# Performance work log

Measured on AMD Instinct MI355X. Metric: run time of the kernel, lower is better.

The kernel has to match this reference:

```python
import jax, jax.numpy as jnp
import numpy as np

# Static problem structure (matches setup_inputs)
B, NPOLY, VPP, L = 32, 256, 64, 32
LAYERS = 3
PLEN = L * 2 ** LAYERS  # 256
LN_EPS = 1e-5


def _layernorm(h, g, b):
    mu = h.mean(-1, keepdims=True)
    var = ((h - mu) ** 2).mean(-1, keepdims=True)
    return g * (h - mu) / jnp.sqrt(var + LN_EPS) + b


def _forward(data, W0, b0, g0, beta0, W1, b1, g1, beta1, W2, b2, g2, beta2,
             Wq, bq, Wk, bk, Wv, bv):
    # row 0 holds agent polyline index in feature 0
    agent_id = data[:, 0, 0].astype(jnp.int32)  # [B]
    vecs = data[:, 1:, :]
    vecs = vecs.at[:, :, -1].set(0.0)  # zero out polyline-id feature (data[:,:,-1]=0)
    x = vecs.reshape(B, NPOLY, VPP, L)  # uniform polyline groups

    # SubGraph: 3 layers of (MLP -> maxpool aggregate -> concat), doubling width
    for (W, b, g, be) in ((W0, b0, g0, beta0), (W1, b1, g1, beta1), (W2, b2, g2, beta2)):
        h = jax.nn.relu(_layernorm(x @ W + b, g, be))  # [B,P,V,c]
        agg = h.max(axis=2, keepdims=True)             # [B,P,1,c]
        x = jnp.concatenate([h, jnp.broadcast_to(agg, h.shape)], axis=-1)  # [B,P,V,2c]
    P = x.max(axis=2)  # [B, NPOLY, PLEN] polyline features

    # Global graph: single-head attention with agent polyline as query
    q = P[jnp.arange(B), agent_id] @ Wq + bq          # [B, C]
    k = P @ Wk + bk                                    # [B, P, C]
    v = P @ Wv + bv
    scores = jnp.einsum('bc,bpc->bp', q, k) / jnp.sqrt(jnp.float32(PLEN))
    att = jax.nn.softmax(scores, axis=-1)
    return jnp.einsum('bp,bpc->bc', att, v)           # [B, PLEN]


def setup_inputs() -> dict:
    key = jax.random.key(0)
    ks = jax.random.split(key, 24)
    V = 1 + NPOLY * VPP
    data = jax.random.normal(ks[0], (B, V, L), dtype=jnp.float32)
    agent = jax.random.randint(ks[1], (B,), 0, NPOLY).astype(jnp.float32)
    data = data.at[:, 0, :].set(0.0).at[:, 0, 0].set(agent)
    pid = jnp.repeat(jnp.arange(NPOLY), VPP).astype(jnp.float32)
    data = data.at[:, 1:, -1].set(pid[None, :])

    inp = {'data': data}
    c = L
    for i in range(LAYERS):
        inp[f'W{i}'] = 0.02 * jax.random.normal(ks[2 + i], (c, c), dtype=jnp.float32)
        inp[f'b{i}'] = jnp.zeros((c,), jnp.float32)
        inp[f'g{i}'] = jnp.ones((c,), jnp.float32)
        inp[f'beta{i}'] = jnp.zeros((c,), jnp.float32)
        c *= 2
    C = PLEN
    for j, nm in enumerate(('q', 'k', 'v')):
        inp[f'W{nm}'] = 0.02 * jax.random.normal(ks[10 + j], (C, C), dtype=jnp.float32)
        inp[f'b{nm}'] = jnp.zeros((C,), jnp.float32)
    return inp


def reference(data, W0, b0, g0, beta0, W1, b1, g1, beta1, W2, b2, g2, beta2,
              Wq, bq, Wk, bk, Wv, bv):
    return _forward(data, W0, b0, g0, beta0, W1, b1, g1, beta1, W2, b2, g2, beta2,
                    Wq, bq, Wk, bk, Wv, bv)
```

## Files before the change

### kernel.cpp

```cpp
#include <hip/hip_runtime.h>

#define NPOLY 256
#define VPP   64
#define LCH   32
#define NV    (1 + NPOLY * VPP)
#define LN_EPS 1e-5f

typedef __bf16 bf16x8 __attribute__((ext_vector_type(8)));
typedef float  f32x4  __attribute__((ext_vector_type(4)));

union U4B8 { uint4 u; bf16x8 v; };

__device__ __forceinline__ unsigned f2bf_u(float f) {
    unsigned u = __float_as_uint(f);
    return (u + 0x7FFFu + ((u >> 16) & 1u)) >> 16;
}
__device__ __forceinline__ unsigned packbf(float a, float b) {
    return f2bf_u(a) | (f2bf_u(b) << 16);
}

__global__ void vn_prep1(const float* __restrict__ W0, const float* __restrict__ W1,
                         const float* __restrict__ W2,
                         const float* __restrict__ Wq, const float* __restrict__ Wk,
                         const float* __restrict__ Wv,
                         float* __restrict__ Wqf, float* __restrict__ Wkf,
                         float* __restrict__ Wvf, uint4* __restrict__ wpack)
{
    int t = blockIdx.x * 256 + threadIdx.x;
    if (t < 3 * 32768) {
        int which = t >> 15, r = t & 32767;
        const float* src = which == 0 ? Wq : which == 1 ? Wk : Wv;
        float*       dst = which == 0 ? Wqf : which == 1 ? Wkf : Wvf;
        dst[r] = src[r] + src[r + 128 * 256];
        return;
    }
    t -= 3 * 32768;
    if (t >= 22 * 64) return;
    int f = t >> 6, L = t & 63, q = L >> 4, m = L & 15;
    const float* src; int N, k0, col;
    if (f < 2)      { src = W0; N = 32;  k0 = q * 8;                 col = f * 16 + m; }
    else if (f < 6) { src = W1; N = 64;  k0 = q * 8;                 col = (f - 2) * 16 + m; }
    else { int g = f - 6; src = W2; N = 128; k0 = (g >> 3) * 32 + q * 8; col = (g & 7) * 16 + m; }
    float e[8];
    #pragma unroll
    for (int j = 0; j < 8; j++) e[j] = src[(k0 + j) * N + col];
    uint4 o;
    o.x = packbf(e[0], e[1]); o.y = packbf(e[2], e[3]);
    o.z = packbf(e[4], e[5]); o.w = packbf(e[6], e[7]);
    wpack[f * 64 + L] = o;
}

__global__ void vn_prep2(const float* __restrict__ Wqf, const float* __restrict__ Wkf,
                         const float* __restrict__ bq,
                         float* __restrict__ Mff, float* __restrict__ u0f)
{
    int t = blockIdx.x * 256 + threadIdx.x;
    if (t < 16384) {
        int i = t >> 7, j = t & 127;
        const float* a = Wqf + i * 256;
        const float* b = Wkf + j * 256;
        float s = 0.f;
        for (int c = 0; c < 256; c++) s = fmaf(a[c], b[c], s);
        Mff[i * 128 + j] = s;
    } else if (t < 16512) {
        int j = t - 16384;
        const float* b = Wkf + j * 256;
        float s = 0.f;
        for (int c = 0; c < 256; c++) s = fmaf(bq[c], b[c], s);
        u0f[j] = s;
    }
}

__global__ __launch_bounds__(64, 2) void vn_mlp(
    const float* __restrict__ data, const uint4* __restrict__ wpack,
    const float* __restrict__ b0, const float* __restrict__ g0, const float* __restrict__ be0,
    const float* __restrict__ W1, const float* __restrict__ b1,
    const float* __restrict__ g1, const float* __restrict__ be1,
    const float* __restrict__ W2, const float* __restrict__ b2,
    const float* __restrict__ g2, const float* __restrict__ be2,
    float* __restrict__ Ph)
{
    __shared__ __align__(16) unsigned short hbuf[64 * 72];
    __shared__ float fbuf[192];

    const int blk = blockIdx.x;
    const int L = threadIdx.x, q = L >> 4, m = L & 15;
    const int bb = blk >> 8, pp = blk & 255;

    const float* rowbase = data + ((size_t)bb * NV + 1 + (size_t)pp * VPP) * LCH;
    bf16x8 A0[4];
    #pragma unroll
    for (int rt = 0; rt < 4; rt++) {
        const float* rp = rowbase + (size_t)(rt * 16 + m) * LCH + q * 8;
        float4 u = *(const float4*)rp;
        float4 v = *(const float4*)(rp + 4);
        if (q == 3) v.w = 0.f;
        U4B8 c;
        c.u.x = packbf(u.x, u.y); c.u.y = packbf(u.z, u.w);
        c.u.z = packbf(v.x, v.y); c.u.w = packbf(v.z, v.w);
        A0[rt] = c.v;
    }
    U4B8 t0, t1; t0.u = wpack[0 * 64 + L]; t1.u = wpack[1 * 64 + L];
    float bc0[2] = { b0[m], b0[16 + m] };
    f32x4 acc0[4][2];
    #pragma unroll
    for (int rt = 0; rt < 4; rt++) {
        {
            f32x4 a = { bc0[0], bc0[0], bc0[0], bc0[0] };
            acc0[rt][0] = __builtin_amdgcn_mfma_f32_16x16x32_bf16(A0[rt], t0.v, a, 0, 0, 0);
        }
        {
            f32x4 a = { bc0[1], bc0[1], bc0[1], bc0[1] };
            acc0[rt][1] = __builtin_amdgcn_mfma_f32_16x16x32_bf16(A0[rt], t1.v, a, 0, 0, 0);
        }
    }
    float g0c[2]  = { g0[m],  g0[16 + m]  };
    float be0c[2] = { be0[m], be0[16 + m] };
    float a0mx[2] = { 0.f, 0.f };
    #pragma unroll
    for (int rt = 0; rt < 4; rt++) {
        #pragma unroll
        for (int reg = 0; reg < 4; reg++) {
            float x0 = acc0[rt][0][reg], x1 = acc0[rt][1][reg];
            float rs = x0 + x1, rq = x0 * x0 + x1 * x1;
            #pragma unroll
            for (int s = 1; s < 16; s <<= 1) { rs += __shfl_xor(rs, s, 64); rq += __shfl_xor(rq, s, 64); }
            float mu = rs * (1.f / 32.f);
            float var = rq * (1.f / 32.f) - mu * mu;
            float ri = rsqrtf(var + LN_EPS);
            #pragma unroll
            for (int ct = 0; ct < 2; ct++) {
                float v = fmaxf(fmaf(g0c[ct] * ri, acc0[rt][ct][reg] - mu, be0c[ct]), 0.f);
                acc0[rt][ct][reg] = v;
                a0mx[ct] = fmaxf(a0mx[ct], v);
            }
        }
    }
    #pragma unroll
    for (int ct = 0; ct < 2; ct++) {
        float v = a0mx[ct];
        v = fmaxf(v, __shfl_xor(v, 16, 64));
        v = fmaxf(v, __shfl_xor(v, 32, 64));
        a0mx[ct] = v;
    }
    if (q == 0) { fbuf[m] = a0mx[0]; fbuf[16 + m] = a0mx[1]; }
    __syncthreads();
    float au1 = b1[L];
    for (int j = 0; j < 32; j++)
        au1 = fmaf(fbuf[j], W1[(32 + j) * 64 + L], au1);
    #pragma unroll
    for (int rt = 0; rt < 4; rt++)
        #pragma unroll
        for (int reg = 0; reg < 4; reg++) {
            int row = rt * 16 + q * 4 + reg;
            hbuf[row * 72 + m]      = (unsigned short)f2bf_u(acc0[rt][0][reg]);
            hbuf[row * 72 + 16 + m] = (unsigned short)f2bf_u(acc0[rt][1][reg]);
        }
    __syncthreads();
    fbuf[64 + L] = au1;
    __syncthreads();

    bf16x8 A1[4];
    #pragma unroll
    for (int rt = 0; rt < 4; rt++) {
        U4B8 c; c.u = *(const uint4*)(hbuf + (rt * 16 + m) * 72 + q * 8);
        A1[rt] = c.v;
    }
    f32x4 acc1[4][4];
    #pragma unroll
    for (int ct = 0; ct < 4; ct++) {
        U4B8 w; w.u = wpack[(2 + ct) * 64 + L];
        float au = fbuf[64 + ct * 16 + m];
        #pragma unroll
        for (int rt = 0; rt < 4; rt++) {
            f32x4 a = { au, au, au, au };
            acc1[rt][ct] = __builtin_amdgcn_mfma_f32_16x16x32_bf16(A1[rt], w.v, a, 0, 0, 0);
        }
    }
    float g1c[4], be1c[4];
    #pragma unroll
    for (int ct = 0; ct < 4; ct++) { g1c[ct] = g1[ct * 16 + m]; be1c[ct] = be1[ct * 16 + m]; }
    float a1mx[4] = { 0.f, 0.f, 0.f, 0.f };
    #pragma unroll
    for (int rt = 0; rt < 4; rt++) {
        #pragma unroll
        for (int reg = 0; reg < 4; reg++) {
            float rs = 0.f, rq = 0.f;
            #pragma unroll
            for (int ct = 0; ct < 4; ct++) { float x = acc1[rt][ct][reg]; rs += x; rq += x * x; }
            #pragma unroll
            for (int s = 1; s < 16; s <<= 1) { rs += __shfl_xor(rs, s, 64); rq += __shfl_xor(rq, s, 64); }
            float mu = rs * (1.f / 64.f);
            float var = rq * (1.f / 64.f) - mu * mu;
            float ri = rsqrtf(var + LN_EPS);
            #pragma unroll
            for (int ct = 0; ct < 4; ct++) {
                float v = fmaxf(fmaf(g1c[ct] * ri, acc1[rt][ct][reg] - mu, be1c[ct]), 0.f);
                acc1[rt][ct][reg] = v;
                a1mx[ct] = fmaxf(a1mx[ct], v);
            }
        }
    }
    #pragma unroll
    for (int ct = 0; ct < 4; ct++) {
        float v = a1mx[ct];
        v = fmaxf(v, __shfl_xor(v, 16, 64));
        v = fmaxf(v, __shfl_xor(v, 32, 64));
        a1mx[ct] = v;
    }
    __syncthreads();
    if (q == 0) {
        #pragma unroll
        for (int ct = 0; ct < 4; ct++) fbuf[ct * 16 + m] = a1mx[ct];
    }
    __syncthreads();
    float au2a = b2[L], au2b = b2[64 + L];
    for (int j = 0; j < 64; j++) {
        float av = fbuf[j];
        au2a = fmaf(av, W2[(64 + j) * 128 + L],      au2a);
        au2b = fmaf(av, W2[(64 + j) * 128 + 64 + L], au2b);
    }
    #pragma unroll
    for (int rt = 0; rt < 4; rt++)
        #pragma unroll
        for (int reg = 0; reg < 4; reg++) {
            int row = rt * 16 + q * 4 + reg;
            #pragma unroll
            for (int ct = 0; ct < 4; ct++)
                hbuf[row * 72 + ct * 16 + m] = (unsigned short)f2bf_u(acc1[rt][ct][reg]);
        }
    __syncthreads();
    fbuf[64 + L] = au2a; fbuf[128 + L] = au2b;
    __syncthreads();

    bf16x8 A2[4][2];
    #pragma unroll
    for (int rt = 0; rt < 4; rt++)
        #pragma unroll
        for (int ks = 0; ks < 2; ks++) {
            U4B8 c; c.u = *(const uint4*)(hbuf + (rt * 16 + m) * 72 + ks * 32 + q * 8);
            A2[rt][ks] = c.v;
        }
    f32x4 acc2[8][4];
    #pragma unroll
    for (int ct = 0; ct < 8; ct++) {
        U4B8 wa, wb;
        wa.u = wpack[(6 + ct) * 64 + L];
        wb.u = wpack[(14 + ct) * 64 + L];
        float au = fbuf[64 + ct * 16 + m];
        #pragma unroll
        for (int rt = 0; rt < 4; rt++) {
            f32x4 a = { au, au, au, au };
            a = __builtin_amdgcn_mfma_f32_16x16x32_bf16(A2[rt][0], wa.v, a, 0, 0, 0);
            a = __builtin_amdgcn_mfma_f32_16x16x32_bf16(A2[rt][1], wb.v, a, 0, 0, 0);
            acc2[ct][rt] = a;
        }
    }
    float g2c[8], be2c[8];
    #pragma unroll
    for (int ct = 0; ct < 8; ct++) { g2c[ct] = g2[ct * 16 + m]; be2c[ct] = be2[ct * 16 + m]; }
    float m2[8] = { 0.f, 0.f, 0.f, 0.f, 0.f, 0.f, 0.f, 0.f };
    #pragma unroll
    for (int rt = 0; rt < 4; rt++) {
        #pragma unroll
        for (int reg = 0; reg < 4; reg++) {
            float rs = 0.f, rq = 0.f;
            #pragma unroll
            for (int ct = 0; ct < 8; ct++) { float x = acc2[ct][rt][reg]; rs += x; rq += x * x; }
            #pragma unroll
            for (int s = 1; s < 16; s <<= 1) { rs += __shfl_xor(rs, s, 64); rq += __shfl_xor(rq, s, 64); }
            float mu = rs * (1.f / 128.f);
            float var = rq * (1.f / 128.f) - mu * mu;
            float ri = rsqrtf(var + LN_EPS);
            #pragma unroll
            for (int ct = 0; ct < 8; ct++) {
                float v = fmaxf(fmaf(g2c[ct] * ri, acc2[ct][rt][reg] - mu, be2c[ct]), 0.f);
                m2[ct] = fmaxf(m2[ct], v);
            }
        }
    }
    #pragma unroll
    for (int ct = 0; ct < 8; ct++) {
        float v = m2[ct];
        v = fmaxf(v, __shfl_xor(v, 16, 64));
        v = fmaxf(v, __shfl_xor(v, 32, 64));
        m2[ct] = v;
    }
    float v1 = q == 0 ? m2[0] : q == 1 ? m2[1] : q == 2 ? m2[2] : m2[3];
    float v2 = q == 0 ? m2[4] : q == 1 ? m2[5] : q == 2 ? m2[6] : m2[7];
    float* op = Ph + (size_t)blk * 128;
    op[L] = v1; op[64 + L] = v2;
}

__global__ __launch_bounds__(256) void vn_attn(
    const float* __restrict__ data, const float* __restrict__ Ph,
    const float* __restrict__ Mff, const float* __restrict__ u0f,
    const float* __restrict__ Wvf, const float* __restrict__ bv,
    float* __restrict__ out)
{
    __shared__ float pah[128], tts[128], sc[256], pb[128], red[8];
    const int b = blockIdx.x, tid = threadIdx.x, lane = tid & 63, wave = tid >> 6;
    const float* PhB = Ph + (size_t)b * NPOLY * 128;
    const int agent = (int)data[(size_t)b * NV * LCH];

    if (tid < 128) pah[tid] = PhB[(size_t)agent * 128 + tid];
    __syncthreads();
    if (tid < 128) {
        float a = u0f[tid];
        for (int i = 0; i < 128; i++) a = fmaf(pah[i], Mff[i * 128 + tid], a);
        tts[tid] = a;
    }
    __syncthreads();
    for (int pi = 0; pi < 64; pi++) {
        const int p = wave * 64 + pi;
        const float* pr = PhB + (size_t)p * 128;
        float s = pr[lane] * tts[lane];
        s = fmaf(pr[64 + lane], tts[64 + lane], s);
        #pragma unroll
        for (int st = 1; st < 64; st <<= 1) s += __shfl_xor(s, st, 64);
        if (lane == 0) sc[p] = s * 0.0625f;
    }
    __syncthreads();
    float sv = sc[tid];
    float mx = sv;
    #pragma unroll
    for (int s = 1; s < 64; s <<= 1) mx = fmaxf(mx, __shfl_xor(mx, s, 64));
    if (lane == 0) red[wave] = mx;
    __syncthreads();
    mx = fmaxf(fmaxf(red[0], red[1]), fmaxf(red[2], red[3]));
    float e = expf(sv - mx);
    float sm = e;
    #pragma unroll
    for (int s = 1; s < 64; s <<= 1) sm += __shfl_xor(sm, s, 64);
    if (lane == 0) red[4 + wave] = sm;
    __syncthreads();
    const float tot = red[4] + red[5] + red[6] + red[7];
    sc[tid] = e / tot;
    __syncthreads();
    if (tid < 128) {
        float a = 0.f;
        for (int p = 0; p < 256; p++) a = fmaf(sc[p], PhB[(size_t)p * 128 + tid], a);
        pb[tid] = a;
    }
    __syncthreads();
    float o = bv[tid];
    for (int j = 0; j < 128; j++) o = fmaf(pb[j], Wvf[j * 256 + tid], o);
    out[(size_t)b * 256 + tid] = o;
}

extern "C" void kernel_launch(void* const* d_in, const int* in_sizes, int n_in,
                              void* d_out, int out_size, void* d_ws, size_t ws_size,
                              hipStream_t stream)
{
    const float* data = (const float*)d_in[0];
    const float* W0 = (const float*)d_in[1];
    const float* b0 = (const float*)d_in[2];
    const float* g0 = (const float*)d_in[3];
    const float* be0= (const float*)d_in[4];
    const float* W1 = (const float*)d_in[5];
    const float* b1 = (const float*)d_in[6];
    const float* g1 = (const float*)d_in[7];
    const float* be1= (const float*)d_in[8];
    const float* W2 = (const float*)d_in[9];
    const float* b2 = (const float*)d_in[10];
    const float* g2 = (const float*)d_in[11];
    const float* be2= (const float*)d_in[12];
    const float* Wq = (const float*)d_in[13];
    const float* bq = (const float*)d_in[14];
    const float* Wk = (const float*)d_in[15];
    const float* bk = (const float*)d_in[16];
    const float* Wv = (const float*)d_in[17];
    const float* bv = (const float*)d_in[18];
    (void)bk;

    char* wsb = (char*)d_ws;
    float* Ph    = (float*)(wsb);
    float* Wqf   = (float*)(wsb + 4194304);
    float* Wkf   = (float*)(wsb + 4325376);
    float* Wvf   = (float*)(wsb + 4456448);
    float* Mff   = (float*)(wsb + 4587520);
    float* u0f   = (float*)(wsb + 4653056);
    uint4* wpack = (uint4*)(wsb + 4653568);

    vn_prep1<<<390, 256, 0, stream>>>(W0, W1, W2, Wq, Wk, Wv, Wqf, Wkf, Wvf, wpack);
    vn_prep2<<<65, 256, 0, stream>>>(Wqf, Wkf, bq, Mff, u0f);
    vn_mlp<<<32 * NPOLY, 64, 0, stream>>>(data, wpack,
                                          b0, g0, be0,
                                          W1, b1, g1, be1,
                                          W2, b2, g2, be2, Ph);
    vn_attn<<<32, 256, 0, stream>>>(data, Ph, Mff, u0f, Wvf, bv, (float*)d_out);
}
```

Measured before the change: 233.5 us.

## Pack four polylines per MLP block and drop the Wq·Wk precompute kernel

```diff
diff --git a/kernel.cpp b/kernel.cpp
--- a/kernel.cpp
+++ b/kernel.cpp
@@ -50,28 +50,7 @@
     wpack[f * 64 + L] = o;
 }
 
-__global__ void vn_prep2(const float* __restrict__ Wqf, const float* __restrict__ Wkf,
-                         const float* __restrict__ bq,
-                         float* __restrict__ Mff, float* __restrict__ u0f)
-{
-    int t = blockIdx.x * 256 + threadIdx.x;
-    if (t < 16384) {
-        int i = t >> 7, j = t & 127;
-        const float* a = Wqf + i * 256;
-        const float* b = Wkf + j * 256;
-        float s = 0.f;
-        for (int c = 0; c < 256; c++) s = fmaf(a[c], b[c], s);
-        Mff[i * 128 + j] = s;
-    } else if (t < 16512) {
-        int j = t - 16384;
-        const float* b = Wkf + j * 256;
-        float s = 0.f;
-        for (int c = 0; c < 256; c++) s = fmaf(bq[c], b[c], s);
-        u0f[j] = s;
-    }
-}
-
-__global__ __launch_bounds__(64, 2) void vn_mlp(
+__global__ __launch_bounds__(256) void vn_mlp(
     const float* __restrict__ data, const uint4* __restrict__ wpack,
     const float* __restrict__ b0, const float* __restrict__ g0, const float* __restrict__ be0,
     const float* __restrict__ W1, const float* __restrict__ b1,
@@ -80,12 +59,16 @@
     const float* __restrict__ g2, const float* __restrict__ be2,
     float* __restrict__ Ph)
 {
-    __shared__ __align__(16) unsigned short hbuf[64 * 72];
-    __shared__ float fbuf[192];
-
-    const int blk = blockIdx.x;
-    const int L = threadIdx.x, q = L >> 4, m = L & 15;
+    __shared__ __align__(16) unsigned short hbuf[4][64 * 72];
+    __shared__ float fbuf[4][192];
+
+    const int w = threadIdx.x >> 6;
+    const int L = threadIdx.x & 63, q = L >> 4, m = L & 15;
+    const int blk = blockIdx.x * 4 + w;
     const int bb = blk >> 8, pp = blk & 255;
+
+    unsigned short* hb = hbuf[w];
+    float* fb = fbuf[w];
 
     const float* rowbase = data + ((size_t)bb * NV + 1 + (size_t)pp * VPP) * LCH;
     bf16x8 A0[4];
@@ -143,38 +126,35 @@
         v = fmaxf(v, __shfl_xor(v, 32, 64));
         a0mx[ct] = v;
     }
-    if (q == 0) { fbuf[m] = a0mx[0]; fbuf[16 + m] = a0mx[1]; }
-    __syncthreads();
+    if (q == 0) { fb[m] = a0mx[0]; fb[16 + m] = a0mx[1]; }
     float au1 = b1[L];
     for (int j = 0; j < 32; j++)
-        au1 = fmaf(fbuf[j], W1[(32 + j) * 64 + L], au1);
+        au1 = fmaf(fb[j], W1[(32 + j) * 64 + L], au1);
     #pragma unroll
     for (int rt = 0; rt < 4; rt++)
         #pragma unroll
         for (int reg = 0; reg < 4; reg++) {
             int row = rt * 16 + q * 4 + reg;
-            hbuf[row * 72 + m]      = (unsigned short)f2bf_u(acc0[rt][0][reg]);
-            hbuf[row * 72 + 16 + m] = (unsigned short)f2bf_u(acc0[rt][1][reg]);
-        }
-    __syncthreads();
-    fbuf[64 + L] = au1;
-    __syncthreads();
+            hb[row * 72 + m]      = (unsigned short)f2bf_u(acc0[rt][0][reg]);
+            hb[row * 72 + 16 + m] = (unsigned short)f2bf_u(acc0[rt][1][reg]);
+        }
+    fb[64 + L] = au1;
 
     bf16x8 A1[4];
     #pragma unroll
     for (int rt = 0; rt < 4; rt++) {
-        U4B8 c; c.u = *(const uint4*)(hbuf + (rt * 16 + m) * 72 + q * 8);
+        U4B8 c; c.u = *(const uint4*)(hb + (rt * 16 + m) * 72 + q * 8);
         A1[rt] = c.v;
     }
     f32x4 acc1[4][4];
     #pragma unroll
     for (int ct = 0; ct < 4; ct++) {
-        U4B8 w; w.u = wpack[(2 + ct) * 64 + L];
-        float au = fbuf[64 + ct * 16 + m];
+        U4B8 wv; wv.u = wpack[(2 + ct) * 64 + L];
+        float au = fb[64 + ct * 16 + m];
         #pragma unroll
         for (int rt = 0; rt < 4; rt++) {
             f32x4 a = { au, au, au, au };
-            acc1[rt][ct] = __builtin_amdgcn_mfma_f32_16x16x32_bf16(A1[rt], w.v, a, 0, 0, 0);
+            acc1[rt][ct] = __builtin_amdgcn_mfma_f32_16x16x32_bf16(A1[rt], wv.v, a, 0, 0, 0);
         }
     }
     float g1c[4], be1c[4];
@@ -208,15 +188,13 @@
         v = fmaxf(v, __shfl_xor(v, 32, 64));
         a1mx[ct] = v;
     }
-    __syncthreads();
     if (q == 0) {
         #pragma unroll
-        for (int ct = 0; ct < 4; ct++) fbuf[ct * 16 + m] = a1mx[ct];
-    }
-    __syncthreads();
+        for (int ct = 0; ct < 4; ct++) fb[ct * 16 + m] = a1mx[ct];
+    }
     float au2a = b2[L], au2b = b2[64 + L];
     for (int j = 0; j < 64; j++) {
-        float av = fbuf[j];
+        float av = fb[j];
         au2a = fmaf(av, W2[(64 + j) * 128 + L],      au2a);
         au2b = fmaf(av, W2[(64 + j) * 128 + 64 + L], au2b);
     }
@@ -227,18 +205,16 @@
             int row = rt * 16 + q * 4 + reg;
             #pragma unroll
             for (int ct = 0; ct < 4; ct++)
-                hbuf[row * 72 + ct * 16 + m] = (unsigned short)f2bf_u(acc1[rt][ct][reg]);
-        }
-    __syncthreads();
-    fbuf[64 + L] = au2a; fbuf[128 + L] = au2b;
-    __syncthreads();
+                hb[row * 72 + ct * 16 + m] = (unsigned short)f2bf_u(acc1[rt][ct][reg]);
+        }
+    fb[64 + L] = au2a; fb[128 + L] = au2b;
 
     bf16x8 A2[4][2];
     #pragma unroll
     for (int rt = 0; rt < 4; rt++)
         #pragma unroll
         for (int ks = 0; ks < 2; ks++) {
-            U4B8 c; c.u = *(const uint4*)(hbuf + (rt * 16 + m) * 72 + ks * 32 + q * 8);
+            U4B8 c; c.u = *(const uint4*)(hb + (rt * 16 + m) * 72 + ks * 32 + q * 8);
             A2[rt][ks] = c.v;
         }
     f32x4 acc2[8][4];
@@ -247,7 +223,7 @@
         U4B8 wa, wb;
         wa.u = wpack[(6 + ct) * 64 + L];
         wb.u = wpack[(14 + ct) * 64 + L];
-        float au = fbuf[64 + ct * 16 + m];
+        float au = fb[64 + ct * 16 + m];
         #pragma unroll
         for (int rt = 0; rt < 4; rt++) {
             f32x4 a = { au, au, au, au };
@@ -294,21 +270,33 @@
 
 __global__ __launch_bounds__(256) void vn_attn(
     const float* __restrict__ data, const float* __restrict__ Ph,
-    const float* __restrict__ Mff, const float* __restrict__ u0f,
-    const float* __restrict__ Wvf, const float* __restrict__ bv,
-    float* __restrict__ out)
+    const float* __restrict__ Wqf, const float* __restrict__ Wkf,
+    const float* __restrict__ Wvf, const float* __restrict__ bq,
+    const float* __restrict__ bv, float* __restrict__ out)
 {
-    __shared__ float pah[128], tts[128], sc[256], pb[128], red[8];
+    __shared__ float pah[128], qs[256], tts[128], sc[256], pb[128], red[8];
     const int b = blockIdx.x, tid = threadIdx.x, lane = tid & 63, wave = tid >> 6;
     const float* PhB = Ph + (size_t)b * NPOLY * 128;
     const int agent = (int)data[(size_t)b * NV * LCH];
 
     if (tid < 128) pah[tid] = PhB[(size_t)agent * 128 + tid];
     __syncthreads();
-    if (tid < 128) {
-        float a = u0f[tid];
-        for (int i = 0; i < 128; i++) a = fmaf(pah[i], Mff[i * 128 + tid], a);
-        tts[tid] = a;
+    {
+        float a = bq[tid];
+        for (int i = 0; i < 128; i++) a = fmaf(pah[i], Wqf[i * 256 + tid], a);
+        qs[tid] = a;
+    }
+    __syncthreads();
+    for (int jj = 0; jj < 32; jj++) {
+        const int j = wave * 32 + jj;
+        const float* wr = Wkf + (size_t)j * 256;
+        float p = wr[lane] * qs[lane];
+        p = fmaf(wr[ 64 + lane], qs[ 64 + lane], p);
+        p = fmaf(wr[128 + lane], qs[128 + lane], p);
+        p = fmaf(wr[192 + lane], qs[192 + lane], p);
+        #pragma unroll
+        for (int s = 1; s < 64; s <<= 1) p += __shfl_xor(p, s, 64);
+        if (lane == 0) tts[j] = p;
     }
     __syncthreads();
     for (int pi = 0; pi < 64; pi++) {
@@ -378,15 +366,12 @@
     float* Wqf   = (float*)(wsb + 4194304);
     float* Wkf   = (float*)(wsb + 4325376);
     float* Wvf   = (float*)(wsb + 4456448);
-    float* Mff   = (float*)(wsb + 4587520);
-    float* u0f   = (float*)(wsb + 4653056);
-    uint4* wpack = (uint4*)(wsb + 4653568);
+    uint4* wpack = (uint4*)(wsb + 4587520);
 
     vn_prep1<<<390, 256, 0, stream>>>(W0, W1, W2, Wq, Wk, Wv, Wqf, Wkf, Wvf, wpack);
-    vn_prep2<<<65, 256, 0, stream>>>(Wqf, Wkf, bq, Mff, u0f);
-    vn_mlp<<<32 * NPOLY, 64, 0, stream>>>(data, wpack,
-                                          b0, g0, be0,
-                                          W1, b1, g1, be1,
-                                          W2, b2, g2, be2, Ph);
-    vn_attn<<<32, 256, 0, stream>>>(data, Ph, Mff, u0f, Wvf, bv, (float*)d_out);
-}
+    vn_mlp<<<2048, 256, 0, stream>>>(data, wpack,
+                                     b0, g0, be0,
+                                     W1, b1, g1, be1,
+                                     W2, b2, g2, be2, Ph);
+    vn_attn<<<32, 256, 0, stream>>>(data, Ph, Wqf, Wkf, Wvf, bq, bv, (float*)d_out);
+}
```

Result: slower. 288.0 us (+23.4%).
